# Performance work log

Hardware: AMD Instinct MI355X
Metric: run time of the kernel (lower is better)

The kernel has to match this reference:

```python
import jax, jax.numpy as jnp
import numpy as np

B, S, D, H = 2, 2048, 1024, 16
DH = D // H
NEG = -1000000000.0


def setup_inputs() -> dict:
    key = jax.random.key(0)
    ks = jax.random.split(key, 8)
    q = jax.random.normal(ks[0], (B, S, D), dtype=jnp.float32)
    k = jax.random.normal(ks[1], (B, S, D), dtype=jnp.float32)
    v = jax.random.normal(ks[2], (B, S, D), dtype=jnp.float32)
    # padding mask [B, k_len]; ensure first key position is valid
    mask = jax.random.randint(ks[3], (B, S), 0, 2, dtype=jnp.int32)
    mask = mask.at[:, 0].set(1)
    scale = 1.0 / np.sqrt(D)
    Wq = jax.random.normal(ks[4], (D, D), dtype=jnp.float32) * scale
    Wk = jax.random.normal(ks[5], (D, D), dtype=jnp.float32) * scale
    Wv = jax.random.normal(ks[6], (D, D), dtype=jnp.float32) * scale
    Wo = jax.random.normal(ks[7], (D, D), dtype=jnp.float32) * scale
    return {"q": q, "k": k, "v": v, "mask": mask,
            "Wq": Wq, "Wk": Wk, "Wv": Wv, "Wo": Wo}


def reference(q, k, v, mask, Wq, Wk, Wv, Wo):
    # nn.Linear(bias=False): y = x @ W.T  (W is [out, in])
    Q = jnp.einsum('bsd,ed->bse', q, Wq)
    K = jnp.einsum('bsd,ed->bse', k, Wk)
    V = jnp.einsum('bsd,ed->bse', v, Wv)
    # split heads -> [B, H, S, DH]
    Q = Q.reshape(B, S, H, DH).transpose(0, 2, 1, 3)
    K = K.reshape(B, S, H, DH).transpose(0, 2, 1, 3)
    V = V.reshape(B, S, H, DH).transpose(0, 2, 1, 3)
    scores = jnp.einsum('bhqd,bhkd->bhqk', Q, K) / jnp.float32(np.sqrt(DH))
    # padding mask: [B, K] -> additive [B, 1, 1, K]
    pad = jnp.where(mask == 0, jnp.float32(NEG), jnp.float32(0.0))[:, None, None, :]
    scores = scores + pad
    # causal (mask_future=True): strict upper triangle blocked
    causal = jnp.where(jnp.triu(jnp.ones((S, S), dtype=bool), k=1),
                       jnp.float32(NEG), jnp.float32(0.0))
    scores = scores + causal
    attn = jax.nn.softmax(scores, axis=-1)
    out = jnp.einsum('bhqk,bhkd->bhqd', attn, V)  # [B, H, S, DH]
    out = out.transpose(0, 2, 1, 3).reshape(B, S, D)
    out = jnp.einsum('bsd,ed->bse', out, Wo)
    # dropout: identity in eval mode
    return out
```

## Files before the change

kernel.cpp:

```cpp
#include <hip/hip_runtime.h>
#include <stdint.h>

#define BB 2
#define SS 2048
#define DD 1024
#define HH 16
#define DHH 64

typedef __bf16 bf16_t;
typedef bf16_t bf16x8 __attribute__((ext_vector_type(8)));
typedef float f32x4 __attribute__((ext_vector_type(4)));
typedef short s16x4 __attribute__((ext_vector_type(4)));

union FragU { uint4 u; bf16x8 b; };
union Frag4U { uint2 u; s16x4 s; };

#if __has_builtin(__builtin_amdgcn_exp2f)
#define EXP2(x) __builtin_amdgcn_exp2f(x)
#else
#define EXP2(x) exp2f(x)
#endif

__device__ __forceinline__ unsigned short f2bf(float f) {
  union { float f; unsigned int u; } x; x.f = f;
  unsigned int u = x.u;
  return (unsigned short)((u + 0x7FFFu + ((u >> 16) & 1u)) >> 16);
}

__device__ __forceinline__ uint2 pack4(float4 v) {
  uint2 r;
  r.x = (unsigned)f2bf(v.x) | ((unsigned)f2bf(v.y) << 16);
  r.y = (unsigned)f2bf(v.z) | ((unsigned)f2bf(v.w) << 16);
  return r;
}

__device__ __forceinline__ uint2 packAcc(f32x4 a) {
  uint2 r;
  r.x = (unsigned)f2bf(a[0]) | ((unsigned)f2bf(a[1]) << 16);
  r.y = (unsigned)f2bf(a[2]) | ((unsigned)f2bf(a[3]) << 16);
  return r;
}

__device__ __forceinline__ bf16x8 ldsFrag(const unsigned short* s, int idx) {
  FragU f;
  f.u = *reinterpret_cast<const uint4*>(s + idx);
  return f.b;
}

__device__ __forceinline__ void gload_lds16(const unsigned short* g, unsigned short* s) {
  __builtin_amdgcn_global_load_lds(
      (const __attribute__((address_space(1))) unsigned int*)g,
      (__attribute__((address_space(3))) unsigned int*)s, 16, 0, 0);
}

#define MFMA16(a, b, c) __builtin_amdgcn_mfma_f32_16x16x32_bf16((a), (b), (c), 0, 0, 0)
#define MFMA16K16(a, b, c) __builtin_amdgcn_mfma_f32_16x16x16bf16_1k((a), (b), (c), 0, 0, 0)

__global__ __launch_bounds__(256) void convert_kernel(
    const float* __restrict__ q, const float* __restrict__ k, const float* __restrict__ v,
    const float* __restrict__ Wq, const float* __restrict__ Wk,
    const float* __restrict__ Wv, const float* __restrict__ Wo,
    const int* __restrict__ mask,
    unsigned short* __restrict__ Ab, unsigned short* __restrict__ Wb,
    float* __restrict__ Mf) {
  const int z = blockIdx.y;
  if (z == 7) {
    if (blockIdx.x >= 4) return;
    const size_t base = (size_t)blockIdx.x * 1024 + (size_t)threadIdx.x * 4;
    int4 m4 = *reinterpret_cast<const int4*>(mask + base);
    float4 p;
    p.x = (m4.x == 0) ? -1.0e9f : 0.0f;
    p.y = (m4.y == 0) ? -1.0e9f : 0.0f;
    p.z = (m4.z == 0) ? -1.0e9f : 0.0f;
    p.w = (m4.w == 0) ? -1.0e9f : 0.0f;
    *reinterpret_cast<float4*>(Mf + base) = p;
    return;
  }
  const float* src;
  unsigned short* dst;
  float scale = 1.0f;
  if (z < 3) {
    src = (z == 0) ? q : (z == 1) ? k : v;
    dst = Ab + (size_t)z * BB * SS * DD;
  } else {
    if (blockIdx.x >= (DD * DD / 1024)) return;
    src = (z == 3) ? Wq : (z == 4) ? Wk : (z == 5) ? Wv : Wo;
    dst = Wb + (size_t)(z - 3) * DD * DD;
    if (z == 3) scale = 0.125f * 1.44269504088896f;
  }
  const size_t base = (size_t)blockIdx.x * 1024 + (size_t)threadIdx.x * 4;
  float4 val = *reinterpret_cast<const float4*>(src + base);
  val.x *= scale; val.y *= scale; val.z *= scale; val.w *= scale;
  uint2 p = pack4(val);
  *reinterpret_cast<uint2*>(dst + base) = p;
}

__global__ __launch_bounds__(256) void proj128_kernel(
    const unsigned short* __restrict__ Ab, const unsigned short* __restrict__ Wb,
    unsigned short* __restrict__ Qb, unsigned short* __restrict__ Kb,
    unsigned short* __restrict__ Vt) {
  __shared__ unsigned short sA[128 * 64];
  __shared__ unsigned short sB[128 * 64];

  const int z = blockIdx.z;
  const unsigned short* A = Ab + (size_t)z * BB * SS * DD;
  const unsigned short* W = Wb + (size_t)z * DD * DD;
  unsigned short* Out = (z == 0) ? Qb : (z == 1) ? Kb : Vt;
  const int layout = (z == 2) ? 1 : 0;

  const int t = threadIdx.x;
  const int lane = t & 63, wave = t >> 6;
  const int quad = lane >> 4, l15 = lane & 15;
  const int wr = wave >> 1, wc = wave & 1;
  const int mBase = blockIdx.x * 128, nBase = blockIdx.y * 128;

  f32x4 acc[4][4] = {};

  for (int k0 = 0; k0 < DD; k0 += 64) {
    #pragma unroll
    for (int i = 0; i < 4; ++i) {
      const int g = wave * 4 + i;
      const int row = g * 8 + (lane >> 3);
      const int oct = (lane & 7) ^ (row & 7);
      gload_lds16(A + (size_t)(mBase + row) * DD + k0 + oct * 8, &sA[g * 512]);
      gload_lds16(W + (size_t)(nBase + row) * DD + k0 + oct * 8, &sB[g * 512]);
    }
    __syncthreads();

    #pragma unroll
    for (int kk = 0; kk < 2; ++kk) {
      bf16x8 af[4], bfr[4];
      #pragma unroll
      for (int i = 0; i < 4; ++i) {
        const int row = wr * 64 + i * 16 + l15;
        af[i] = ldsFrag(sA, (row * 8 + ((kk * 4 + quad) ^ (l15 & 7))) * 8);
      }
      #pragma unroll
      for (int j = 0; j < 4; ++j) {
        const int row = wc * 64 + j * 16 + l15;
        bfr[j] = ldsFrag(sB, (row * 8 + ((kk * 4 + quad) ^ (l15 & 7))) * 8);
      }
      if (layout == 0) {
        #pragma unroll
        for (int i = 0; i < 4; ++i)
          #pragma unroll
          for (int j = 0; j < 4; ++j)
            acc[i][j] = MFMA16(bfr[j], af[i], acc[i][j]);
      } else {
        #pragma unroll
        for (int i = 0; i < 4; ++i)
          #pragma unroll
          for (int j = 0; j < 4; ++j)
            acc[i][j] = MFMA16(af[i], bfr[j], acc[i][j]);
      }
    }
    __syncthreads();
  }

  const int b = mBase >> 11;
  const int sbase = mBase & (SS - 1);
  if (layout == 0) {
    #pragma unroll
    for (int i = 0; i < 4; ++i) {
      #pragma unroll
      for (int j = 0; j < 4; ++j) {
        const int s = sbase + wr * 64 + i * 16 + l15;
        const int n = nBase + wc * 64 + j * 16 + quad * 4;
        const int h = n >> 6, dh = n & (DHH - 1);
        uint2 w = packAcc(acc[i][j]);
        *reinterpret_cast<uint2*>(
            Out + ((size_t)(b * HH + h) * SS + s) * DHH + dh) = w;
      }
    }
  } else {
    #pragma unroll
    for (int i = 0; i < 4; ++i) {
      #pragma unroll
      for (int j = 0; j < 4; ++j) {
        const int s = sbase + wr * 64 + i * 16 + quad * 4;
        const int n = nBase + wc * 64 + j * 16 + l15;
        const int h = n >> 6, dh = n & (DHH - 1);
        uint2 w = packAcc(acc[i][j]);
        *reinterpret_cast<uint2*>(
            Out + ((size_t)(b * HH + h) * DHH + dh) * SS + s) = w;
      }
    }
  }
}

__global__ __launch_bounds__(256, 4) void attn_kernel(
    const unsigned short* __restrict__ Qb, const unsigned short* __restrict__ Kb,
    const unsigned short* __restrict__ Vt, const float* __restrict__ Mf,
    unsigned short* __restrict__ Obh) {
  __shared__ __align__(16) unsigned short sK[2][64 * 64];
  __shared__ __align__(16) unsigned short sV[2][64 * 64];
  unsigned short* sO = &sK[0][0];

  const int t = threadIdx.x;
  const int lane = t & 63, wave = t >> 6;
  const int quad = lane >> 4, l15 = lane & 15;

  const int id = blockIdx.x;
  const int xcd = id & 7, rest = id >> 3;
  const int hg = rest >> 5;
  const int hd = xcd * 4 + hg;
  const int r5 = rest & 31;
  const int qt = (hg & 1) ? (31 - r5) : r5;
  const int b = hd >> 4;
  const int qb = qt * 64;

  const size_t headOff = (size_t)hd * SS * DHH;
  const unsigned short* Qh = Qb + headOff;
  const unsigned short* Kh = Kb + headOff;
  const unsigned short* Vh = Vt + headOff;
  const float* Mp = Mf + b * SS;

  bf16x8 aq[2];
  {
    const unsigned short* qp = Qh + (size_t)(qb + wave * 16 + l15) * DHH + quad * 8;
    FragU f0, f1;
    f0.u = *reinterpret_cast<const uint4*>(qp);
    f1.u = *reinterpret_cast<const uint4*>(qp + 32);
    aq[0] = f0.b; aq[1] = f1.b;
  }

  const int srow = lane >> 3, soct = lane & 7;

  #pragma unroll
  for (int i = 0; i < 2; ++i) {
    const int g = wave * 2 + i;
    const int row = g * 8 + srow;
    const int oct = soct ^ (row & 7);
    gload_lds16(Kh + (size_t)row * DHH + oct * 8, &sK[0][g * 512]);
    gload_lds16(Vh + (size_t)row * SS + oct * 8, &sV[0][g * 512]);
  }

  float m_l = -1.0e30f, l_l = 0.0f;
  f32x4 oacc[4] = {};
  const int qrow_abs = qb + wave * 16 + l15;

  for (int c = 0; c <= qt; ++c) {
    __syncthreads();
    if (c < qt) {
      const int c1 = (c + 1) * 64;
      const int nb = (c + 1) & 1;
      #pragma unroll
      for (int i = 0; i < 2; ++i) {
        const int g = wave * 2 + i;
        const int row = g * 8 + srow;
        const int oct = soct ^ (row & 7);
        gload_lds16(Kh + (size_t)(c1 + row) * DHH + oct * 8, &sK[nb][g * 512]);
        gload_lds16(Vh + (size_t)row * SS + c1 + oct * 8, &sV[nb][g * 512]);
      }
    }
    const int cb = c & 1;
    const int c0 = c * 64;

    f32x4 sacc[4] = {};
    #pragma unroll
    for (int kk = 0; kk < 2; ++kk) {
      #pragma unroll
      for (int j = 0; j < 4; ++j) {
        const int row = j * 16 + l15;
        bf16x8 ak = ldsFrag(sK[cb], (row * 8 + ((kk * 4 + quad) ^ (l15 & 7))) * 8);
        sacc[j] = MFMA16(ak, aq[kk], sacc[j]);
      }
    }

    float rm = -1.0e30f;
    #pragma unroll
    for (int j = 0; j < 4; ++j)
      rm = fmaxf(rm, fmaxf(fmaxf(sacc[j][0], sacc[j][1]), fmaxf(sacc[j][2], sacc[j][3])));
    rm = fmaxf(rm, __shfl_xor(rm, 16));
    rm = fmaxf(rm, __shfl_xor(rm, 32));
    const float mnew = fmaxf(m_l, rm);
    const float alpha = EXP2(m_l - mnew);
    m_l = mnew;

    const bool diag = (c == qt);
    float rs = 0.0f;
    s16x4 pk[4];
    #pragma unroll
    for (int j = 0; j < 4; ++j) {
      float4 pf = *reinterpret_cast<const float4*>(Mp + c0 + j * 16 + quad * 4);
      float p0 = EXP2(sacc[j][0] - mnew + pf.x);
      float p1 = EXP2(sacc[j][1] - mnew + pf.y);
      float p2 = EXP2(sacc[j][2] - mnew + pf.z);
      float p3 = EXP2(sacc[j][3] - mnew + pf.w);
      if (diag) {
        const int key = c0 + j * 16 + quad * 4;
        p0 = (key + 0 > qrow_abs) ? 0.0f : p0;
        p1 = (key + 1 > qrow_abs) ? 0.0f : p1;
        p2 = (key + 2 > qrow_abs) ? 0.0f : p2;
        p3 = (key + 3 > qrow_abs) ? 0.0f : p3;
      }
      rs += (p0 + p1) + (p2 + p3);
      Frag4U fu;
      fu.u.x = __builtin_amdgcn_perm(__float_as_uint(p1) + 0x8000u,
                                     __float_as_uint(p0) + 0x8000u, 0x07060302u);
      fu.u.y = __builtin_amdgcn_perm(__float_as_uint(p3) + 0x8000u,
                                     __float_as_uint(p2) + 0x8000u, 0x07060302u);
      pk[j] = fu.s;
    }
    rs += __shfl_xor(rs, 16);
    rs += __shfl_xor(rs, 32);
    l_l = l_l * alpha + rs;

    #pragma unroll
    for (int jn = 0; jn < 4; ++jn)
      oacc[jn] *= alpha;

    #pragma unroll
    for (int j = 0; j < 4; ++j) {
      #pragma unroll
      for (int jn = 0; jn < 4; ++jn) {
        const int row = jn * 16 + l15;
        const int oct = (2 * j + (quad >> 1)) ^ (l15 & 7);
        Frag4U av;
        av.u = *reinterpret_cast<const uint2*>(&sV[cb][(row * 8 + oct) * 8 + (quad & 1) * 4]);
        oacc[jn] = MFMA16K16(av.s, pk[j], oacc[jn]);
      }
    }
  }

  __syncthreads();
  const float inv = 1.0f / l_l;
  #pragma unroll
  for (int jn = 0; jn < 4; ++jn) {
    uint2 w;
    w.x = (unsigned)f2bf(oacc[jn][0] * inv) | ((unsigned)f2bf(oacc[jn][1] * inv) << 16);
    w.y = (unsigned)f2bf(oacc[jn][2] * inv) | ((unsigned)f2bf(oacc[jn][3] * inv) << 16);
    *reinterpret_cast<uint2*>(&sO[(wave * 16 + l15) * 72 + jn * 16 + quad * 4]) = w;
  }
  __syncthreads();
  {
    const int row = t >> 2, seg = t & 3;
    uint4 u0 = *reinterpret_cast<const uint4*>(&sO[row * 72 + seg * 16]);
    uint4 u1 = *reinterpret_cast<const uint4*>(&sO[row * 72 + seg * 16 + 8]);
    unsigned short* dst = Obh + headOff + (size_t)(qb + row) * DHH + seg * 16;
    *reinterpret_cast<uint4*>(dst) = u0;
    *reinterpret_cast<uint4*>(dst + 8) = u1;
  }
}

__global__ __launch_bounds__(256) void outproj_kernel(
    const unsigned short* __restrict__ Obh, const unsigned short* __restrict__ Wb,
    float* __restrict__ Out) {
  __shared__ unsigned short sA[2][128 * 64];
  __shared__ unsigned short sB[2][128 * 64];

  const unsigned short* W = Wb + (size_t)3 * DD * DD;
  const int t = threadIdx.x;
  const int lane = t & 63, wave = t >> 6;
  const int quad = lane >> 4, l15 = lane & 15;
  const int wr = wave >> 1, wc = wave & 1;
  const int mBase = blockIdx.x * 128, nBase = blockIdx.y * 128;
  const int srow = lane >> 3, soct = lane & 7;

  const int bidx = mBase >> 11;
  const int sloc = mBase & (SS - 1);
  const unsigned short* Abase = Obh + (size_t)bidx * HH * SS * DHH;

  f32x4 acc[4][4] = {};

  #pragma unroll
  for (int i = 0; i < 4; ++i) {
    const int g = wave * 4 + i;
    const int row = g * 8 + srow;
    const int oct = soct ^ (row & 7);
    gload_lds16(Abase + ((size_t)0 * SS + sloc + row) * DHH + oct * 8, &sA[0][g * 512]);
    gload_lds16(W + (size_t)(nBase + row) * DD + oct * 8, &sB[0][g * 512]);
  }

  for (int kt = 0; kt < HH; ++kt) {
    __syncthreads();
    if (kt + 1 < HH) {
      const int nb = (kt + 1) & 1;
      #pragma unroll
      for (int i = 0; i < 4; ++i) {
        const int g = wave * 4 + i;
        const int row = g * 8 + srow;
        const int oct = soct ^ (row & 7);
        gload_lds16(Abase + ((size_t)(kt + 1) * SS + sloc + row) * DHH + oct * 8,
                    &sA[nb][g * 512]);
        gload_lds16(W + (size_t)(nBase + row) * DD + (kt + 1) * 64 + oct * 8,
                    &sB[nb][g * 512]);
      }
    }
    const int cb = kt & 1;
    #pragma unroll
    for (int kk = 0; kk < 2; ++kk) {
      bf16x8 af[4], bfr[4];
      #pragma unroll
      for (int i = 0; i < 4; ++i) {
        const int row = wr * 64 + i * 16 + l15;
        af[i] = ldsFrag(sA[cb], (row * 8 + ((kk * 4 + quad) ^ (l15 & 7))) * 8);
      }
      #pragma unroll
      for (int j = 0; j < 4; ++j) {
        const int row = wc * 64 + j * 16 + l15;
        bfr[j] = ldsFrag(sB[cb], (row * 8 + ((kk * 4 + quad) ^ (l15 & 7))) * 8);
      }
      #pragma unroll
      for (int i = 0; i < 4; ++i)
        #pragma unroll
        for (int j = 0; j < 4; ++j)
          acc[i][j] = MFMA16(bfr[j], af[i], acc[i][j]);
    }
  }

  #pragma unroll
  for (int i = 0; i < 4; ++i) {
    #pragma unroll
    for (int j = 0; j < 4; ++j) {
      const int m = mBase + wr * 64 + i * 16 + l15;
      const int n = nBase + wc * 64 + j * 16 + quad * 4;
      float4 w;
      w.x = acc[i][j][0]; w.y = acc[i][j][1];
      w.z = acc[i][j][2]; w.w = acc[i][j][3];
      *reinterpret_cast<float4*>(Out + (size_t)m * DD + n) = w;
    }
  }
}

extern "C" void kernel_launch(void* const* d_in, const int* in_sizes, int n_in,
                              void* d_out, int out_size, void* d_ws, size_t ws_size,
                              hipStream_t stream) {
  (void)in_sizes; (void)n_in; (void)out_size; (void)ws_size;
  const float* q  = (const float*)d_in[0];
  const float* k  = (const float*)d_in[1];
  const float* v  = (const float*)d_in[2];
  const int* mask = (const int*)d_in[3];
  const float* Wq = (const float*)d_in[4];
  const float* Wk = (const float*)d_in[5];
  const float* Wv = (const float*)d_in[6];
  const float* Wo = (const float*)d_in[7];
  float* out = (float*)d_out;

  const size_t AE = (size_t)BB * SS * DD;
  unsigned short* Ab  = (unsigned short*)d_ws;
  unsigned short* Obh = Ab;
  unsigned short* Wb  = Ab + 3 * AE;
  unsigned short* Qb  = Wb + (size_t)4 * DD * DD;
  unsigned short* Kb  = Qb + AE;
  unsigned short* Vt  = Kb + AE;
  float* Mf = (float*)(Vt + AE);

  convert_kernel<<<dim3(AE / 1024, 8), 256, 0, stream>>>(
      q, k, v, Wq, Wk, Wv, Wo, mask, Ab, Wb, Mf);

  proj128_kernel<<<dim3(BB * SS / 128, DD / 128, 3), 256, 0, stream>>>(
      Ab, Wb, Qb, Kb, Vt);

  attn_kernel<<<dim3(32 * HH * BB), 256, 0, stream>>>(Qb, Kb, Vt, Mf, Obh);

  outproj_kernel<<<dim3(BB * SS / 128, DD / 128), 256, 0, stream>>>(Obh, Wb, out);
}
```

Measured before the change: 225.9 us.

## Software-pipeline QK^T one chunk ahead with triple-buffered K tiles

Triple-buffers the K tiles in LDS and prefetches K two chunks ahead. The QK^T MFMAs for the next chunk are computed before the softmax of the current chunk, so score computation can overlap the exp/softmax work. It also skips the alpha rescale of the accumulators when the running max does not change (wave-uniform check) and raises wave priority around the MFMA sections. The cost is more LDS per block and more live registers, which may lower occupancy under the 256x4 launch bounds.

```diff
diff --git a/kernel.cpp b/kernel.cpp
--- a/kernel.cpp
+++ b/kernel.cpp
@@ -192,7 +192,7 @@
     const unsigned short* __restrict__ Qb, const unsigned short* __restrict__ Kb,
     const unsigned short* __restrict__ Vt, const float* __restrict__ Mf,
     unsigned short* __restrict__ Obh) {
-  __shared__ __align__(16) unsigned short sK[2][64 * 64];
+  __shared__ __align__(16) unsigned short sK[3][64 * 64];
   __shared__ __align__(16) unsigned short sV[2][64 * 64];
   unsigned short* sO = &sK[0][0];
 
@@ -234,94 +234,150 @@
     gload_lds16(Kh + (size_t)row * DHH + oct * 8, &sK[0][g * 512]);
     gload_lds16(Vh + (size_t)row * SS + oct * 8, &sV[0][g * 512]);
   }
+  if (qt >= 1) {
+    #pragma unroll
+    for (int i = 0; i < 2; ++i) {
+      const int g = wave * 2 + i;
+      const int row = g * 8 + srow;
+      const int oct = soct ^ (row & 7);
+      gload_lds16(Kh + (size_t)(64 + row) * DHH + oct * 8, &sK[1][g * 512]);
+    }
+  }
 
   float m_l = -1.0e30f, l_l = 0.0f;
   f32x4 oacc[4] = {};
   const int qrow_abs = qb + wave * 16 + l15;
-
-  for (int c = 0; c <= qt; ++c) {
-    __syncthreads();
-    if (c < qt) {
-      const int c1 = (c + 1) * 64;
-      const int nb = (c + 1) & 1;
-      #pragma unroll
-      for (int i = 0; i < 2; ++i) {
-        const int g = wave * 2 + i;
-        const int row = g * 8 + srow;
-        const int oct = soct ^ (row & 7);
-        gload_lds16(Kh + (size_t)(c1 + row) * DHH + oct * 8, &sK[nb][g * 512]);
-        gload_lds16(Vh + (size_t)row * SS + c1 + oct * 8, &sV[nb][g * 512]);
-      }
-    }
-    const int cb = c & 1;
-    const int c0 = c * 64;
-
-    f32x4 sacc[4] = {};
-    #pragma unroll
-    for (int kk = 0; kk < 2; ++kk) {
-      #pragma unroll
-      for (int j = 0; j < 4; ++j) {
-        const int row = j * 16 + l15;
-        bf16x8 ak = ldsFrag(sK[cb], (row * 8 + ((kk * 4 + quad) ^ (l15 & 7))) * 8);
-        sacc[j] = MFMA16(ak, aq[kk], sacc[j]);
-      }
-    }
-
-    float rm = -1.0e30f;
-    #pragma unroll
-    for (int j = 0; j < 4; ++j)
-      rm = fmaxf(rm, fmaxf(fmaxf(sacc[j][0], sacc[j][1]), fmaxf(sacc[j][2], sacc[j][3])));
-    rm = fmaxf(rm, __shfl_xor(rm, 16));
-    rm = fmaxf(rm, __shfl_xor(rm, 32));
-    const float mnew = fmaxf(m_l, rm);
-    const float alpha = EXP2(m_l - mnew);
-    m_l = mnew;
-
-    const bool diag = (c == qt);
-    float rs = 0.0f;
-    s16x4 pk[4];
-    #pragma unroll
-    for (int j = 0; j < 4; ++j) {
-      float4 pf = *reinterpret_cast<const float4*>(Mp + c0 + j * 16 + quad * 4);
-      float p0 = EXP2(sacc[j][0] - mnew + pf.x);
-      float p1 = EXP2(sacc[j][1] - mnew + pf.y);
-      float p2 = EXP2(sacc[j][2] - mnew + pf.z);
-      float p3 = EXP2(sacc[j][3] - mnew + pf.w);
-      if (diag) {
-        const int key = c0 + j * 16 + quad * 4;
-        p0 = (key + 0 > qrow_abs) ? 0.0f : p0;
-        p1 = (key + 1 > qrow_abs) ? 0.0f : p1;
-        p2 = (key + 2 > qrow_abs) ? 0.0f : p2;
-        p3 = (key + 3 > qrow_abs) ? 0.0f : p3;
-      }
-      rs += (p0 + p1) + (p2 + p3);
-      Frag4U fu;
-      fu.u.x = __builtin_amdgcn_perm(__float_as_uint(p1) + 0x8000u,
-                                     __float_as_uint(p0) + 0x8000u, 0x07060302u);
-      fu.u.y = __builtin_amdgcn_perm(__float_as_uint(p3) + 0x8000u,
-                                     __float_as_uint(p2) + 0x8000u, 0x07060302u);
-      pk[j] = fu.s;
-    }
-    rs += __shfl_xor(rs, 16);
-    rs += __shfl_xor(rs, 32);
-    l_l = l_l * alpha + rs;
-
-    #pragma unroll
-    for (int jn = 0; jn < 4; ++jn)
-      oacc[jn] *= alpha;
-
-    #pragma unroll
-    for (int j = 0; j < 4; ++j) {
-      #pragma unroll
-      for (int jn = 0; jn < 4; ++jn) {
-        const int row = jn * 16 + l15;
-        const int oct = (2 * j + (quad >> 1)) ^ (l15 & 7);
-        Frag4U av;
-        av.u = *reinterpret_cast<const uint2*>(&sV[cb][(row * 8 + oct) * 8 + (quad & 1) * 4]);
-        oacc[jn] = MFMA16K16(av.s, pk[j], oacc[jn]);
-      }
-    }
-  }
+  const f32x4 zero4 = {};
+  f32x4 sacc_a[4], sacc_b[4];
+
+  int kc = 0, kn = 1, ks = 2;
+
+#define QK_CHUNK(DST, SLOT)                                                     \
+  {                                                                             \
+    _Pragma("unroll")                                                           \
+    for (int j = 0; j < 4; ++j) {                                               \
+      const int row = j * 16 + l15;                                             \
+      bf16x8 ak0 = ldsFrag(sK[SLOT], (row * 8 + (quad ^ (l15 & 7))) * 8);       \
+      bf16x8 ak1 = ldsFrag(sK[SLOT], (row * 8 + ((4 + quad) ^ (l15 & 7))) * 8); \
+      f32x4 tmp = MFMA16(ak0, aq[0], zero4);                                    \
+      DST[j] = MFMA16(ak1, aq[1], tmp);                                         \
+    }                                                                           \
+  }
+
+#define ATTN_ITER(CUR, NXT)                                                     \
+  {                                                                             \
+    __syncthreads();                                                            \
+    if (c + 2 <= qt) {                              \
+      const int c2 = (c + 2) * 64;                                              \
+      _Pragma("unroll")                                                         \
+      for (int i = 0; i < 2; ++i) {                                             \
+        const int g = wave * 2 + i;                                             \
+        const int row = g * 8 + srow;                                           \
+        const int oct = soct ^ (row & 7);                                       \
+        gload_lds16(Kh + (size_t)(c2 + row) * DHH + oct * 8, &sK[ks][g * 512]); \
+      }                                                                         \
+    }                                                                           \
+    if (c + 1 <= qt) {                         \
+      const int c1 = (c + 1) * 64;                                              \
+      const int nb = (c + 1) & 1;                                               \
+      _Pragma("unroll")                                                         \
+      for (int i = 0; i < 2; ++i) {                                             \
+        const int g = wave * 2 + i;                                             \
+        const int row = g * 8 + srow;                                           \
+        const int oct = soct ^ (row & 7);                                       \
+        gload_lds16(Vh + (size_t)row * SS + c1 + oct * 8, &sV[nb][g * 512]);    \
+      }                                                                         \
+    }                                                                           \
+    const int c0 = c * 64;                                                      \
+    float4 pf0 = *reinterpret_cast<const float4*>(Mp + c0 + quad * 4);          \
+    float4 pf1 = *reinterpret_cast<const float4*>(Mp + c0 + 16 + quad * 4);     \
+    float4 pf2 = *reinterpret_cast<const float4*>(Mp + c0 + 32 + quad * 4);     \
+    float4 pf3 = *reinterpret_cast<const float4*>(Mp + c0 + 48 + quad * 4);     \
+    if (c == 0) { QK_CHUNK(CUR, 0) }                   \
+    __builtin_amdgcn_s_setprio(1);                                              \
+    if (c < qt) { QK_CHUNK(NXT, kn) }            \
+    __builtin_amdgcn_s_setprio(0);                                              \
+                             \
+    float rm = -1.0e30f;                                                        \
+    _Pragma("unroll")                                                           \
+    for (int j = 0; j < 4; ++j)                                                 \
+      rm = fmaxf(rm, fmaxf(fmaxf(CUR[j][0], CUR[j][1]),                         \
+                           fmaxf(CUR[j][2], CUR[j][3])));                       \
+    rm = fmaxf(rm, __shfl_xor(rm, 16));                                         \
+    rm = fmaxf(rm, __shfl_xor(rm, 32));                                         \
+    float mnew;                                                                 \
+    if (__all(rm <= m_l)) {                                                     \
+      mnew = m_l;                         \
+    } else {                                                                    \
+      mnew = fmaxf(m_l, rm);                                                    \
+      const float alpha = EXP2(m_l - mnew);                                     \
+      m_l = mnew;                                                               \
+      _Pragma("unroll")                                                         \
+      for (int jn = 0; jn < 4; ++jn) oacc[jn] *= alpha;                         \
+      l_l *= alpha;                                                             \
+    }                                                                           \
+    const bool diag = (c == qt);                                                \
+    float rs = 0.0f;                                                            \
+    s16x4 pk[4];                                                                \
+    {                                                                           \
+      const float4 pfa[4] = {pf0, pf1, pf2, pf3};                               \
+      _Pragma("unroll")                                                         \
+      for (int j = 0; j < 4; ++j) {                                             \
+        float p0 = EXP2(CUR[j][0] - mnew + pfa[j].x);                           \
+        float p1 = EXP2(CUR[j][1] - mnew + pfa[j].y);                           \
+        float p2 = EXP2(CUR[j][2] - mnew + pfa[j].z);                           \
+        float p3 = EXP2(CUR[j][3] - mnew + pfa[j].w);                           \
+        if (diag) {                                                             \
+          const int key = c0 + j * 16 + quad * 4;                               \
+          p0 = (key + 0 > qrow_abs) ? 0.0f : p0;                                \
+          p1 = (key + 1 > qrow_abs) ? 0.0f : p1;                                \
+          p2 = (key + 2 > qrow_abs) ? 0.0f : p2;                                \
+          p3 = (key + 3 > qrow_abs) ? 0.0f : p3;                                \
+        }                                                                       \
+        rs += (p0 + p1) + (p2 + p3);                                            \
+        Frag4U fu;                                                              \
+        fu.u.x = __builtin_amdgcn_perm(__float_as_uint(p1) + 0x8000u,           \
+                                       __float_as_uint(p0) + 0x8000u,           \
+                                       0x07060302u);                            \
+        fu.u.y = __builtin_amdgcn_perm(__float_as_uint(p3) + 0x8000u,           \
+                                       __float_as_uint(p2) + 0x8000u,           \
+                                       0x07060302u);                            \
+        pk[j] = fu.s;                                                           \
+      }                                                                         \
+    }                                                                           \
+    rs += __shfl_xor(rs, 16);                                                   \
+    rs += __shfl_xor(rs, 32);                                                   \
+    l_l += rs;                                                                  \
+                                                      \
+    const int cb = c & 1;                                                       \
+    __builtin_amdgcn_s_setprio(1);                                              \
+    _Pragma("unroll")                                                           \
+    for (int j = 0; j < 4; ++j) {                                               \
+      _Pragma("unroll")                                                         \
+      for (int jn = 0; jn < 4; ++jn) {                                          \
+        const int row = jn * 16 + l15;                                          \
+        const int oct = (2 * j + (quad >> 1)) ^ (l15 & 7);                      \
+        Frag4U av;                                                              \
+        av.u = *reinterpret_cast<const uint2*>(                                 \
+            &sV[cb][(row * 8 + oct) * 8 + (quad & 1) * 4]);                     \
+        oacc[jn] = MFMA16K16(av.s, pk[j], oacc[jn]);                            \
+      }                                                                         \
+    }                                                                           \
+    __builtin_amdgcn_s_setprio(0);                                              \
+  }
+
+  int c = 0;
+  while (true) {
+    ATTN_ITER(sacc_a, sacc_b)
+    if (c == qt) break;
+    ++c; { const int t0 = kc; kc = kn; kn = ks; ks = t0; }
+    ATTN_ITER(sacc_b, sacc_a)
+    if (c == qt) break;
+    ++c; { const int t0 = kc; kc = kn; kn = ks; ks = t0; }
+  }
+
+#undef ATTN_ITER
+#undef QK_CHUNK
 
   __syncthreads();
   const float inv = 1.0f / l_l;
```

After: 231.6 us. +2.5%, slower.
